# Kernel optimization log

Hardware: AMD Instinct MI355X
Metric: run time of the kernel (lower is better)

The kernel has to match this reference:

```python
import jax, jax.numpy as jnp
import numpy as np

K = 3
STRIDE = 1
PAD = 1
DIL = 1


def _unfold(a):
    # a: (N, C, H, W) -> patches (N, C, K*K, oH, oW), matching torch.F.unfold
    # channel-major ordering (c slowest, then kernel row, then kernel col).
    N, C, H, W = a.shape
    oH = (H + 2 * PAD - DIL * (K - 1) - 1) // STRIDE + 1
    oW = (W + 2 * PAD - DIL * (K - 1) - 1) // STRIDE + 1
    ap = jnp.pad(a, ((0, 0), (0, 0), (PAD, PAD), (PAD, PAD)))
    cols = []
    for i in range(K):
        for j in range(K):
            cols.append(ap[:, :,
                           i * DIL: i * DIL + (oH - 1) * STRIDE + 1: STRIDE,
                           j * DIL: j * DIL + (oW - 1) * STRIDE + 1: STRIDE])
    return jnp.stack(cols, axis=2)  # (N, C, K*K, oH, oW)


def setup_inputs() -> dict:
    key = jax.random.key(0)
    k1, k2, k3, k4, k5 = jax.random.split(key, 5)
    N, C, O, H, W = 4, 128, 256, 128, 128
    x = jax.random.normal(k1, (N, C, H, W), dtype=jnp.float32)
    depth = jax.random.uniform(k2, (N, 1, H, W), dtype=jnp.float32)
    camera_params = jax.random.normal(k3, (N, 4), dtype=jnp.float32)
    weight = jax.random.normal(k4, (O, C, K, K), dtype=jnp.float32) * 0.05
    bias = jax.random.normal(k5, (O,), dtype=jnp.float32) * 0.05
    return {"x": x, "depth": depth, "camera_params": camera_params,
            "weight": weight, "bias": bias}


def reference(x, depth, camera_params, weight, bias):
    # camera_params is accepted but unused, mirroring the torch module.
    O, C = weight.shape[0], weight.shape[1]
    xp = _unfold(x)        # (N, C, kk, oH, oW)
    dp = _unfold(depth)    # (N, 1, kk, oH, oW)
    w = weight.reshape(O, C, K * K)
    # depth-modulated im2col GEMM: sum_{c,p} w[o,c,p] * x_patch * d_patch
    out = jnp.einsum('ocp,ncpxy->noxy', w, xp * dp)
    return out + bias[None, :, None, None]
```

## Files before the change

kernel.cpp:

```cpp
#include <hip/hip_runtime.h>
#include <stdint.h>


#define C_IN 128
#define O_OUT 256
#define HW 128
#define NB 4
#define PADW 130

#define XD_ELEMS ((size_t)NB * PADW * PADW * C_IN)
#define XD_BYTES (XD_ELEMS * 2)
#define WT_ELEMS ((size_t)O_OUT * C_IN * 9)
#define WT_BYTES (WT_ELEMS * 2)

typedef __attribute__((ext_vector_type(8))) short short8;
typedef __attribute__((ext_vector_type(4))) float f32x4;
typedef __attribute__((ext_vector_type(4))) unsigned uint4v;

__device__ __forceinline__ unsigned f2bf_bits(float f) {
  unsigned u = __builtin_bit_cast(unsigned, f);
  return (u + 0x7fffu + ((u >> 16) & 1u)) >> 16;
}

__device__ __forceinline__ void async_load16(const void* g, void* l) {
  __builtin_amdgcn_global_load_lds(
      (__attribute__((address_space(1))) void*)g,
      (__attribute__((address_space(3))) void*)l, 16, 0, 0);
}

__global__ __launch_bounds__(256) void prep_xd(const float* __restrict__ x,
                                               const float* __restrict__ depth,
                                               short* __restrict__ xd) {
  __shared__ short s[128 * 130];

  const int R = blockIdx.x;
  if (R >= NB * HW) {
    const int n = R - NB * HW;
    uint4v* base0 = (uint4v*)(xd + (size_t)n * PADW * PADW * C_IN);
    uint4v* base1 = (uint4v*)(xd + ((size_t)n * PADW + (PADW - 1)) * PADW * C_IN);
    const uint4v z = {0u, 0u, 0u, 0u};
    const int per_row = PADW * C_IN * 2 / 16;
    for (int i = threadIdx.x; i < per_row; i += 256) {
      base0[i] = z;
      base1[i] = z;
    }
    return;
  }

  const int n = R >> 7, y = R & 127;
  const int tid = threadIdx.x;
  const int lane = tid & 63;
  const int wave = tid >> 6;

  {
    unsigned* row = (unsigned*)(xd + ((size_t)(n * PADW + y + 1) * PADW) * C_IN);
    if (tid < 64) row[tid] = 0u;
    else if (tid < 128) row[(size_t)(PADW - 1) * 64 + (tid - 64)] = 0u;
  }

  typedef __attribute__((ext_vector_type(2))) float f32x2;
  const f32x2 d2 = *(const f32x2*)(depth + ((size_t)n * HW + y) * HW + 2 * lane);
  const float* xrow = x + (((size_t)n * C_IN) * HW + y) * HW + 2 * lane;
#pragma unroll 8
  for (int ci = 0; ci < 32; ++ci) {
    const int c = ci * 4 + wave;
    const f32x2 v = *(const f32x2*)(xrow + (size_t)c * HW * HW);
    s[(2 * lane) * 130 + c] = (short)f2bf_bits(v.x * d2.x);
    s[(2 * lane + 1) * 130 + c] = (short)f2bf_bits(v.y * d2.y);
  }
  __syncthreads();

  unsigned* orow = (unsigned*)(xd + ((size_t)(n * PADW + y + 1) * PADW + 1) * C_IN);
#pragma unroll 8
  for (int i = 0; i < 32; ++i) {
    const int flat = tid + i * 256;
    const int px = flat >> 6, cp = flat & 63;
    orow[flat] = ((const unsigned*)s)[px * 65 + cp];
  }
}

__global__ void prep_wt(const float* __restrict__ w, short* __restrict__ wt) {
  const int gid = blockIdx.x * 256 + threadIdx.x;
  if (gid >= (int)WT_ELEMS) return;
  const int c = gid & 127;
  const int tap = (gid >> 7) % 9;
  const int o = gid / (9 * 128);
  wt[gid] = (short)f2bf_bits(w[((size_t)o * C_IN + c) * 9 + tap]);
}

__global__ __launch_bounds__(256) void conv_mfma(
    const short* __restrict__ xd, const short* __restrict__ wt,
    const float* __restrict__ bias, float* __restrict__ out) {
  __shared__ short lds[16384];

  const int tid = threadIdx.x;
  const int R = blockIdx.x;
  const int n = R >> 7, y = R & 127;
  const int o0 = blockIdx.y << 7;
  const int lane = tid & 63;
  const int wave = tid >> 6;
  const int wm = wave & 1, wn = wave >> 1;
  const int ln = lane & 15, q = lane >> 4;

  const int row0 = tid >> 2;
  const int part = (tid & 3) ^ (row0 & 3);

  const short* wg0 = wt + (size_t)(o0 + row0) * 1152 + part * 8;
  const short* wg1 = wt + (size_t)(o0 + row0 + 64) * 1152 + part * 8;
  const short* xg0 = xd + ((size_t)(n * PADW + y) * PADW + row0) * C_IN + part * 8;
  const short* xg1 = xg0 + (size_t)64 * C_IN;

  f32x4 acc[4][4] = {};

  auto stage = [&](int kt, int bufo) {
    const int tap = kt >> 2;
    const int cc = kt & 3;
    const int ti = tap / 3;
    const int tj = tap - ti * 3;
    const int wofs = kt << 5;
    const int xofs = ((ti * PADW + tj) << 7) + (cc << 5);
    short* lb = lds + bufo + tid * 8;
    async_load16(wg0 + wofs, lb);
    async_load16(wg1 + wofs, lb + 2048);
    async_load16(xg0 + xofs, lb + 4096);
    async_load16(xg1 + xofs, lb + 6144);
  };

  stage(0, 0);

  const int swz = (ln & 3);

  for (int kt = 0; kt < 36; ++kt) {
    __syncthreads();

    if (kt + 1 < 36) stage(kt + 1, ((kt + 1) & 1) << 13);

    const short* Ws = lds + ((kt & 1) << 13);
    const short* Xs = Ws + 4096;

    short8 a[4], b[4];
#pragma unroll
    for (int t = 0; t < 4; ++t)
      a[t] = *(const short8*)(Ws + (((wm << 6) + (t << 4) + ln) << 5) +
                              ((q ^ swz) << 3));
#pragma unroll
    for (int u = 0; u < 4; ++u)
      b[u] = *(const short8*)(Xs + (((wn << 6) + (u << 4) + ln) << 5) +
                              ((q ^ swz) << 3));
#pragma unroll
    for (int t = 0; t < 4; ++t)
#pragma unroll
      for (int u = 0; u < 4; ++u)
        acc[t][u] =
            __builtin_amdgcn_mfma_f32_16x16x32_bf16(a[t], b[u], acc[t][u], 0, 0, 0);
  }

#pragma unroll
  for (int t = 0; t < 4; ++t) {
    const int ob = o0 + (wm << 6) + (t << 4) + (q << 2);
#pragma unroll
    for (int u = 0; u < 4; ++u) {
      const int xcol = (wn << 6) + (u << 4) + ln;
#pragma unroll
      for (int r = 0; r < 4; ++r) {
        const int o = ob + r;
        out[(((size_t)n * O_OUT + o) * HW + y) * HW + xcol] = acc[t][u][r] + bias[o];
      }
    }
  }
}

__global__ void conv_naive(const float* __restrict__ x,
                           const float* __restrict__ depth,
                           const float* __restrict__ w,
                           const float* __restrict__ bias,
                           float* __restrict__ out) {
  const int gid = blockIdx.x * 256 + threadIdx.x;
  if (gid >= NB * O_OUT * HW * HW) return;
  const int xc = gid & 127;
  const int y = (gid >> 7) & 127;
  const int o = (gid >> 14) & 255;
  const int n = gid >> 22;
  float s = bias[o];
  for (int c = 0; c < C_IN; ++c)
    for (int i = 0; i < 3; ++i) {
      const int yy = y + i - 1;
      if (yy < 0 || yy >= HW) continue;
      for (int j = 0; j < 3; ++j) {
        const int xx = xc + j - 1;
        if (xx < 0 || xx >= HW) continue;
        s += w[((o * C_IN + c) * 3 + i) * 3 + j] *
             x[(((size_t)n * C_IN + c) * HW + yy) * HW + xx] *
             depth[((size_t)n * HW + yy) * HW + xx];
      }
    }
  out[gid] = s;
}

extern "C" void kernel_launch(void* const* d_in, const int* in_sizes, int n_in,
                              void* d_out, int out_size, void* d_ws, size_t ws_size,
                              hipStream_t stream) {
  const float* x = (const float*)d_in[0];
  const float* depth = (const float*)d_in[1];
  const float* weight = (const float*)d_in[3];
  const float* bias = (const float*)d_in[4];
  float* out = (float*)d_out;

  const size_t need = XD_BYTES + WT_BYTES;
  if (ws_size < need) {
    conv_naive<<<(NB * O_OUT * HW * HW + 255) / 256, 256, 0, stream>>>(
        x, depth, weight, bias, out);
    return;
  }

  short* xd = (short*)d_ws;
  short* wt = (short*)((char*)d_ws + XD_BYTES);

  prep_xd<<<NB * HW + NB, 256, 0, stream>>>(x, depth, xd);
  prep_wt<<<(int)((WT_ELEMS + 255) / 256), 256, 0, stream>>>(weight, wt);
  conv_mfma<<<dim3(NB * HW, 2), 256, 0, stream>>>(xd, wt, bias, out);
}
```

Measured before the change: 157.0 us.

## Compute two output rows per block to double weight-tile reuse

Each conv block now covers two output rows (256 pixels) rather than one, so every 128-wide weight tile loaded into LDS is reused across twice as many pixels. Each wave now holds a 4x8 MFMA accumulator tile, the double-buffered LDS staging grows to six async loads per step, and the grid is halved. The XOR swizzle on LDS reads and writes is also removed, which may bring back bank conflicts. Register pressure rises from the doubled accumulators, with launch bounds set to two blocks per CU.

```diff
diff --git a/kernel.cpp b/kernel.cpp
--- a/kernel.cpp
+++ b/kernel.cpp
@@ -88,14 +88,15 @@
   wt[gid] = (short)f2bf_bits(w[((size_t)o * C_IN + c) * 9 + tap]);
 }
 
-__global__ __launch_bounds__(256) void conv_mfma(
+__global__ __launch_bounds__(256, 2) void conv_mfma(
     const short* __restrict__ xd, const short* __restrict__ wt,
     const float* __restrict__ bias, float* __restrict__ out) {
-  __shared__ short lds[16384];
+  __shared__ short lds[24576];
 
   const int tid = threadIdx.x;
-  const int R = blockIdx.x;
-  const int n = R >> 7, y = R & 127;
+  const int bx = blockIdx.x;
+  const int n = bx >> 6;
+  const int y = (bx & 63) << 1;
   const int o0 = blockIdx.y << 7;
   const int lane = tid & 63;
   const int wave = tid >> 6;
@@ -103,54 +104,53 @@
   const int ln = lane & 15, q = lane >> 4;
 
   const int row0 = tid >> 2;
-  const int part = (tid & 3) ^ (row0 & 3);
+  const int part = tid & 3;
 
   const short* wg0 = wt + (size_t)(o0 + row0) * 1152 + part * 8;
-  const short* wg1 = wt + (size_t)(o0 + row0 + 64) * 1152 + part * 8;
-  const short* xg0 = xd + ((size_t)(n * PADW + y) * PADW + row0) * C_IN + part * 8;
-  const short* xg1 = xg0 + (size_t)64 * C_IN;
-
-  f32x4 acc[4][4] = {};
-
-  auto stage = [&](int kt, int bufo) {
+  const short* wg1 = wg0 + (size_t)64 * 1152;
+  const short* xh0 = xd + ((size_t)(n * PADW + y) * PADW + row0) * C_IN + part * 8;
+  const short* xh1 = xh0 + (size_t)PADW * C_IN;
+
+  f32x4 acc[4][8] = {};
+
+  auto stage = [&](int kt) {
     const int tap = kt >> 2;
     const int cc = kt & 3;
     const int ti = tap / 3;
     const int tj = tap - ti * 3;
-    const int wofs = kt << 5;
-    const int xofs = ((ti * PADW + tj) << 7) + (cc << 5);
-    short* lb = lds + bufo + tid * 8;
-    async_load16(wg0 + wofs, lb);
-    async_load16(wg1 + wofs, lb + 2048);
-    async_load16(xg0 + xofs, lb + 4096);
-    async_load16(xg1 + xofs, lb + 6144);
+    const int wo = kt << 5;
+    const int xo = (ti * PADW + tj) * C_IN + (cc << 5);
+    short* lb = lds + ((kt & 1) ? 12288 : 0) + tid * 8;
+    async_load16(wg0 + wo, lb);
+    async_load16(wg1 + wo, lb + 2048);
+    async_load16(xh0 + xo, lb + 4096);
+    async_load16(xh0 + 64 * C_IN + xo, lb + 6144);
+    async_load16(xh1 + xo, lb + 8192);
+    async_load16(xh1 + 64 * C_IN + xo, lb + 10240);
   };
 
-  stage(0, 0);
-
-  const int swz = (ln & 3);
-
+  stage(0);
+
+#pragma unroll 4
   for (int kt = 0; kt < 36; ++kt) {
     __syncthreads();
 
-    if (kt + 1 < 36) stage(kt + 1, ((kt + 1) & 1) << 13);
-
-    const short* Ws = lds + ((kt & 1) << 13);
+    if (kt + 1 < 36) stage(kt + 1);
+
+    const short* Ws = lds + ((kt & 1) ? 12288 : 0);
     const short* Xs = Ws + 4096;
 
-    short8 a[4], b[4];
+    short8 a[4], b[8];
 #pragma unroll
     for (int t = 0; t < 4; ++t)
-      a[t] = *(const short8*)(Ws + (((wm << 6) + (t << 4) + ln) << 5) +
-                              ((q ^ swz) << 3));
-#pragma unroll
-    for (int u = 0; u < 4; ++u)
-      b[u] = *(const short8*)(Xs + (((wn << 6) + (u << 4) + ln) << 5) +
-                              ((q ^ swz) << 3));
+      a[t] = *(const short8*)(Ws + (((wm << 6) + (t << 4) + ln) << 5) + (q << 3));
+#pragma unroll
+    for (int u = 0; u < 8; ++u)
+      b[u] = *(const short8*)(Xs + (((wn << 7) + (u << 4) + ln) << 5) + (q << 3));
 #pragma unroll
     for (int t = 0; t < 4; ++t)
 #pragma unroll
-      for (int u = 0; u < 4; ++u)
+      for (int u = 0; u < 8; ++u)
         acc[t][u] =
             __builtin_amdgcn_mfma_f32_16x16x32_bf16(a[t], b[u], acc[t][u], 0, 0, 0);
   }
@@ -159,12 +159,14 @@
   for (int t = 0; t < 4; ++t) {
     const int ob = o0 + (wm << 6) + (t << 4) + (q << 2);
 #pragma unroll
-    for (int u = 0; u < 4; ++u) {
-      const int xcol = (wn << 6) + (u << 4) + ln;
+    for (int u = 0; u < 8; ++u) {
+      const int xcol = (u << 4) + ln;
+      const int yrow = y + wn;
 #pragma unroll
       for (int r = 0; r < 4; ++r) {
         const int o = ob + r;
-        out[(((size_t)n * O_OUT + o) * HW + y) * HW + xcol] = acc[t][u][r] + bias[o];
+        out[(((size_t)n * O_OUT + o) * HW + yrow) * HW + xcol] =
+            acc[t][u][r] + bias[o];
       }
     }
   }
@@ -218,5 +220,5 @@
 
   prep_xd<<<NB * HW + NB, 256, 0, stream>>>(x, depth, xd);
   prep_wt<<<(int)((WT_ELEMS + 255) / 256), 256, 0, stream>>>(weight, wt);
-  conv_mfma<<<dim3(NB * HW, 2), 256, 0, stream>>>(xd, wt, bias, out);
-}
+  conv_mfma<<<dim3(NB * HW / 2, 2), 256, 0, stream>>>(xd, wt, bias, out);
+}
```

New measurement: 139.9 us. 1.12x faster.
